# Kernel optimization log

Measured on AMD Instinct MI355X. Metric: run time of the kernel, lower is better.

Reference implementation:

```python
import jax, jax.numpy as jnp
import numpy as np

K = 2  # DGL TAGConv default number of hops
N_GRAPHS = 64


def _tag_conv(h, src, dst, W, b, norm):
    # TAGConv: concat [h, A_hat h, A_hat^2 h] @ W + b, A_hat = D^-1/2 A D^-1/2
    n = h.shape[0]
    hops = [h]
    cur = h
    for _ in range(K):
        msg = (cur * norm)[src]                      # gather from src, [E, d]
        agg = jnp.zeros_like(cur).at[dst].add(msg)   # scatter-sum to dst
        cur = agg * norm
        hops.append(cur)
    z = jnp.concatenate(hops, axis=-1)               # [N, (K+1)*d]
    return jax.nn.relu(z @ W + b)


def _norm(dst, n):
    deg = jnp.zeros((n,), jnp.float32).at[dst].add(1.0)
    deg = jnp.clip(deg, 1.0, None)
    return (deg ** -0.5)[:, None]                    # [N, 1]


def setup_inputs() -> dict:
    key = jax.random.key(0)
    ks = jax.random.split(key, 8)
    N, E, IN, HID, C = 100000, 3200000, 128, 256, 10
    h = jax.random.normal(ks[0], (N, IN), jnp.float32)
    src = jax.random.randint(ks[1], (E,), 0, N, jnp.int32)
    dst = jax.random.randint(ks[2], (E,), 0, N, jnp.int32)
    graph_ids = jnp.sort(jax.random.randint(ks[3], (N,), 0, N_GRAPHS, jnp.int32))
    s1 = ((K + 1) * IN) ** -0.5
    s2 = ((K + 1) * HID) ** -0.5
    W1 = jax.random.normal(ks[4], ((K + 1) * IN, HID), jnp.float32) * s1
    b1 = jnp.zeros((HID,), jnp.float32)
    W2 = jax.random.normal(ks[5], ((K + 1) * HID, HID), jnp.float32) * s2
    b2 = jnp.zeros((HID,), jnp.float32)
    Wc = jax.random.normal(ks[6], (HID, C), jnp.float32) * (HID ** -0.5)
    bc = jnp.zeros((C,), jnp.float32)
    return {"h": h, "src": src, "dst": dst, "graph_ids": graph_ids,
            "W1": W1, "b1": b1, "W2": W2, "b2": b2, "Wc": Wc, "bc": bc}


def reference(h, src, dst, graph_ids, W1, b1, W2, b2, Wc, bc):
    n = h.shape[0]
    norm = _norm(dst, n)
    x = _tag_conv(h, src, dst, W1, b1, norm)
    x = _tag_conv(x, src, dst, W2, b2, norm)
    pooled = jax.ops.segment_max(x, graph_ids, num_segments=N_GRAPHS)  # [G, HID]
    return pooled @ Wc + bc                                            # [G, C]
```

## Files before the change

### kernel.cpp

```cpp
#include <hip/hip_runtime.h>
#include <hip/hip_bf16.h>


typedef unsigned short u16;
typedef unsigned int u32;
typedef unsigned char u8;

__device__ inline float u2f(u16 u) { return __uint_as_float(((u32)u) << 16); }
__device__ inline u16 f2u(float f) {
    __hip_bfloat16 b = __float2bfloat16(f);
    return *reinterpret_cast<u16*>(&b);
}


constexpr int NPB = 128, NC = 128, NBMAX = 784;

__global__ __launch_bounds__(256) void countA_kernel(
    const int* __restrict__ dst, int* __restrict__ Hmat, int E, int CS, int NB) {
    __shared__ int hist[NBMAX];
    int tid = threadIdx.x;
    for (int b = tid; b < NB; b += 256) hist[b] = 0;
    __syncthreads();
    int base = blockIdx.x * CS;
    int end = base + CS < E ? base + CS : E;
    for (int i = base + tid; i < end; i += 256) {
        int d = __builtin_nontemporal_load(dst + i);
        atomicAdd(&hist[d >> 7], 1);
    }
    __syncthreads();
    for (int b = tid; b < NB; b += 256) Hmat[b * NC + blockIdx.x] = hist[b];
}

__global__ __launch_bounds__(256) void scatterC_kernel(
    const int* __restrict__ src, const int* __restrict__ dst,
    const int* __restrict__ Omat, uint2* __restrict__ Earr,
    int E, int CS, int NB) {
    __shared__ int cur[NBMAX];
    int tid = threadIdx.x;
    int c = blockIdx.x;
    for (int b = tid; b < NB; b += 256) cur[b] = Omat[b * NC + c];
    __syncthreads();
    int base = c * CS;
    int end = base + CS < E ? base + CS : E;
    for (int i = base + tid; i < end; i += 256) {
        int d = __builtin_nontemporal_load(dst + i);
        int s = __builtin_nontemporal_load(src + i);
        int pos = atomicAdd(&cur[d >> 7], 1);
        uint2 e;
        e.x = (u32)s;
        e.y = (u32)(d & (NPB - 1));
        Earr[pos] = e;
    }
}

__global__ __launch_bounds__(256) void fineD_kernel(
    const uint2* __restrict__ Earr, const int* __restrict__ Omat,
    int* __restrict__ colidx, int* __restrict__ rowptr,
    float* __restrict__ normv, int N, int E, int NB) {
    __shared__ int cnt[NPB];
    __shared__ int scn[NPB];
    __shared__ int cur2[NPB];
    int tid = threadIdx.x;
    int b = blockIdx.x;
    int base = Omat[b * NC];
    int end = Omat[(b + 1) * NC];
    if (tid < NPB) cnt[tid] = 0;
    __syncthreads();
    for (int i = base + tid; i < end; i += 256)
        atomicAdd(&cnt[Earr[i].y], 1);
    __syncthreads();
    if (tid < NPB) scn[tid] = cnt[tid];
    __syncthreads();
    for (int off = 1; off < NPB; off <<= 1) {
        int v = (tid < NPB && tid >= off) ? scn[tid - off] : 0;
        __syncthreads();
        if (tid < NPB) scn[tid] += v;
        __syncthreads();
    }
    int node0 = b * NPB;
    if (tid < NPB) {
        int excl = scn[tid] - cnt[tid];
        cur2[tid] = base + excl;
        int node = node0 + tid;
        if (node < N) {
            rowptr[node] = base + excl;
            int d = cnt[tid];
            float fd = d < 1 ? 1.0f : (float)d;
            normv[node] = rsqrtf(fd);
        }
    }
    if (b == 0 && tid == 0) rowptr[N] = E;
    __syncthreads();
    for (int i = base + tid; i < end; i += 256) {
        uint2 e = Earr[i];
        int pos = atomicAdd(&cur2[e.y], 1);
        colidx[pos] = (int)e.x;
    }
}

__global__ void scan1_kernel(const int* __restrict__ in, int* __restrict__ outp,
                             int* __restrict__ bsum, int n) {
    __shared__ int sd[1024];
    int t = threadIdx.x;
    int i = blockIdx.x * 1024 + t;
    int v = (i < n) ? in[i] : 0;
    sd[t] = v;
    __syncthreads();
    for (int off = 1; off < 1024; off <<= 1) {
        int x = (t >= off) ? sd[t - off] : 0;
        __syncthreads();
        sd[t] += x;
        __syncthreads();
    }
    if (i < n) outp[i] = sd[t] - v;
    if (t == 1023) bsum[blockIdx.x] = sd[t];
}

__global__ void scan2_kernel(int* __restrict__ bsum, int nb) {
    __shared__ int sd[1024];
    int t = threadIdx.x;
    int v = (t < nb) ? bsum[t] : 0;
    sd[t] = v;
    __syncthreads();
    for (int off = 1; off < 1024; off <<= 1) {
        int x = (t >= off) ? sd[t - off] : 0;
        __syncthreads();
        sd[t] += x;
        __syncthreads();
    }
    if (t < nb) bsum[t] = sd[t] - v;
}

__global__ void scan3_kernel(int* __restrict__ outp, const int* __restrict__ bsum,
                             int n, int E) {
    int i = blockIdx.x * blockDim.x + threadIdx.x;
    if (i < n) outp[i] += bsum[i >> 10];
    if (i == 0) outp[n] = E;
}


struct alignas(4) U2 { u16 v[2]; };
struct alignas(8) U4 { u16 v[4]; };
struct alignas(16) U8 { u16 v[8]; };


__global__ __launch_bounds__(256) void castquant_f32_128(
    const float* __restrict__ h, u16* __restrict__ cat, int ldcat,
    const float* __restrict__ normv,
    u8* __restrict__ q, float* __restrict__ m, int N) {
    int row = blockIdx.x * 4 + (threadIdx.x >> 6);
    if (row >= N) return;
    int lane = threadIdx.x & 63;
    float2 f = *(const float2*)(h + (size_t)row * 128 + lane * 2);
    U2 o;
    o.v[0] = f2u(f.x);
    o.v[1] = f2u(f.y);
    *(U2*)(cat + (size_t)row * ldcat + lane * 2) = o;
    float mx = fmaxf(fabsf(f.x), fabsf(f.y));
    #pragma unroll
    for (int off = 32; off > 0; off >>= 1)
        mx = fmaxf(mx, __shfl_xor(mx, off, 64));
    float inv = mx > 0.f ? 127.f / mx : 0.f;
    u32 q0 = (u32)((int)rintf(f.x * inv) + 128);
    u32 q1 = (u32)((int)rintf(f.y * inv) + 128);
    *(unsigned short*)(q + (size_t)row * 128 + lane * 2) =
        (unsigned short)(q0 | (q1 << 8));
    if (lane == 0) m[row] = normv[row] * (mx * (1.f / 127.f));
}


__global__ __launch_bounds__(256) void quant_bf16_256(
    const u16* __restrict__ x, const float* __restrict__ normv,
    u8* __restrict__ q, float* __restrict__ m, int N) {
    int row = blockIdx.x * 4 + (threadIdx.x >> 6);
    if (row >= N) return;
    int lane = threadIdx.x & 63;
    U4 v = *(const U4*)(x + (size_t)row * 256 + lane * 4);
    float f[4];
    #pragma unroll
    for (int i = 0; i < 4; ++i) f[i] = u2f(v.v[i]);
    float mx = fmaxf(fmaxf(fabsf(f[0]), fabsf(f[1])),
                     fmaxf(fabsf(f[2]), fabsf(f[3])));
    #pragma unroll
    for (int off = 32; off > 0; off >>= 1)
        mx = fmaxf(mx, __shfl_xor(mx, off, 64));
    float inv = mx > 0.f ? 127.f / mx : 0.f;
    u32 b0 = (u32)((int)rintf(f[0] * inv) + 128);
    u32 b1 = (u32)((int)rintf(f[1] * inv) + 128);
    u32 b2 = (u32)((int)rintf(f[2] * inv) + 128);
    u32 b3 = (u32)((int)rintf(f[3] * inv) + 128);
    *(u32*)(q + (size_t)row * 256 + lane * 4) =
        b0 | (b1 << 8) | (b2 << 16) | (b3 << 24);
    if (lane == 0) m[row] = normv[row] * (mx * (1.f / 127.f));
}


template <int BPL, int QOUT>
__global__ __launch_bounds__(256, 2) void prop_q8_kernel(
    const u8* __restrict__ qin, const float* __restrict__ m,
    u16* __restrict__ out, int ldout,
    const int* __restrict__ rowptr, const int* __restrict__ colidx,
    const float* __restrict__ normv, int N,
    u8* __restrict__ qout, float* __restrict__ mout) {
    constexpr int D = 32 * BPL;
    constexpr int NW = BPL / 4;
    constexpr int UE = 8;
    int node = blockIdx.x * 4 + (threadIdx.x >> 6);
    if (node >= N) return;
    const int lane = threadIdx.x & 63;
    const int half = lane >> 5;
    const int l32 = lane & 31;
    const u32 laneoff = (u32)l32 * BPL;
    int s = rowptr[node], e = rowptr[node + 1];
    float acc[BPL];
    #pragma unroll
    for (int q = 0; q < BPL; ++q) acc[q] = 0.f;
    float msum = 0.f;
    const int nfull = (e - s) >> 4;
    int p = s;
    if (nfull > 0) {
        int c[UE];
        #pragma unroll
        for (int u = 0; u < UE; ++u) c[u] = colidx[s + 2 * u + half];
        for (int g = 0; g < nfull; ++g) {
            u32 w[UE][NW];
            #pragma unroll
            for (int u = 0; u < UE; ++u) {
                u32 off = (u32)c[u] * D + laneoff;
                if (BPL == 8) {
                    uint2 gg = *(const uint2*)(qin + off);
                    w[u][0] = gg.x; w[u][1] = gg.y;
                } else {
                    w[u][0] = *(const u32*)(qin + off);
                }
            }
            float nm[UE];
            #pragma unroll
            for (int u = 0; u < UE; ++u) nm[u] = m[c[u]];
            if (g + 1 < nfull) {
                int pn = s + (g + 1) * 16;
                #pragma unroll
                for (int u = 0; u < UE; ++u) c[u] = colidx[pn + 2 * u + half];
            }
            #pragma unroll
            for (int u = 0; u < UE; ++u) {
                msum += nm[u];
                #pragma unroll
                for (int t = 0; t < NW; ++t) {
                    u32 ww = w[u][t];
                    acc[4 * t + 0] += nm[u] * (float)(ww & 0xffu);
                    acc[4 * t + 1] += nm[u] * (float)((ww >> 8) & 0xffu);
                    acc[4 * t + 2] += nm[u] * (float)((ww >> 16) & 0xffu);
                    acc[4 * t + 3] += nm[u] * (float)(ww >> 24);
                }
            }
        }
        p = s + nfull * 16;
    }
    if (p < e) {
        const int el = e - 1;
        int c[UE];
        #pragma unroll
        for (int u = 0; u < UE; ++u) {
            int idx = p + 2 * u + half;
            c[u] = colidx[idx < e ? idx : el];
        }
        u32 w[UE][NW];
        #pragma unroll
        for (int u = 0; u < UE; ++u) {
            u32 off = (u32)c[u] * D + laneoff;
            if (BPL == 8) {
                uint2 gg = *(const uint2*)(qin + off);
                w[u][0] = gg.x; w[u][1] = gg.y;
            } else {
                w[u][0] = *(const u32*)(qin + off);
            }
        }
        float nm[UE];
        #pragma unroll
        for (int u = 0; u < UE; ++u) {
            int idx = p + 2 * u + half;
            float mm = m[c[u]];
            nm[u] = idx < e ? mm : 0.f;
        }
        #pragma unroll
        for (int u = 0; u < UE; ++u) {
            msum += nm[u];
            #pragma unroll
            for (int t = 0; t < NW; ++t) {
                u32 ww = w[u][t];
                acc[4 * t + 0] += nm[u] * (float)(ww & 0xffu);
                acc[4 * t + 1] += nm[u] * (float)((ww >> 8) & 0xffu);
                acc[4 * t + 2] += nm[u] * (float)((ww >> 16) & 0xffu);
                acc[4 * t + 3] += nm[u] * (float)(ww >> 24);
            }
        }
    }
    #pragma unroll
    for (int q = 0; q < BPL; ++q) acc[q] += __shfl_xor(acc[q], 32, 64);
    msum += __shfl_xor(msum, 32, 64);
    float nn = normv[node];
    #pragma unroll
    for (int q = 0; q < BPL; ++q) acc[q] = nn * (acc[q] - 128.f * msum);
    if (half == 0) {
        if (BPL == 8) {
            U8 o;
            #pragma unroll
            for (int q = 0; q < 8; ++q) o.v[q] = f2u(acc[q]);
            *(U8*)(out + (size_t)node * ldout + l32 * 8) = o;
        } else {
            U4 o;
            #pragma unroll
            for (int q = 0; q < 4; ++q) o.v[q] = f2u(acc[q]);
            *(U4*)(out + (size_t)node * ldout + l32 * 4) = o;
        }
    }
    if (QOUT) {
        float mx = 0.f;
        #pragma unroll
        for (int q = 0; q < BPL; ++q) mx = fmaxf(mx, fabsf(acc[q]));
        #pragma unroll
        for (int off = 16; off > 0; off >>= 1)
            mx = fmaxf(mx, __shfl_xor(mx, off, 64));
        float inv = mx > 0.f ? 127.f / mx : 0.f;
        if (half == 0) {
            u32 b[BPL > 4 ? 8 : 4];
            #pragma unroll
            for (int q = 0; q < BPL; ++q)
                b[q] = (u32)((int)rintf(acc[q] * inv) + 128);
            if (BPL == 8) {
                uint2 g;
                g.x = b[0] | (b[1] << 8) | (b[2] << 16) | (b[3] << 24);
                g.y = b[4] | (b[5] << 8) | (b[6] << 16) | (b[7] << 24);
                *(uint2*)(qout + (size_t)node * D + l32 * 8) = g;
            } else {
                *(u32*)(qout + (size_t)node * D + l32 * 4) =
                    b[0] | (b[1] << 8) | (b[2] << 16) | (b[3] << 24);
            }
            if (lane == 0) mout[node] = nn * (mx * (1.f / 127.f));
        }
    }
}


typedef __attribute__((ext_vector_type(8))) short bf16x8f;
typedef __attribute__((ext_vector_type(4))) float f32x4;

template <int KK>
__global__ __launch_bounds__(256, 3) void gemm_wave(
    const u16* __restrict__ A,
    const u16* __restrict__ Bt,
    const u16* __restrict__ Cadd,
    const float* __restrict__ bias,
    u16* __restrict__ Cout,
    int M, int NJOBS, int relu) {
    const int tid = threadIdx.x;
    const int lane = tid & 63;
    const int wave = tid >> 6;
    int nwg = gridDim.x;
    int qq = nwg >> 3, rr = nwg & 7;
    int xcd = blockIdx.x & 7, wi = blockIdx.x >> 3;
    int slot = (xcd < rr ? xcd * (qq + 1) : rr * (qq + 1) + (xcd - rr) * qq) + wi;
    int job = slot * 4 + wave;
    if (job >= NJOBS) return;
    const int rt = job >> 3;
    const int cg = job & 7;
    const int row0 = rt << 7;
    const int col0 = cg << 5;
    const int mb = lane & 15;
    const int seg = lane >> 4;
    const int NOUT = 256;

    const u16* pA = A + (size_t)(row0 + mb) * KK + seg * 8;
    const u16* pB = Bt + (size_t)(col0 + mb) * KK + seg * 8;

    f32x4 acc[8][2];
    #pragma unroll
    for (int mi = 0; mi < 8; ++mi) {
        acc[mi][0] = (f32x4)0.f;
        acc[mi][1] = (f32x4)0.f;
    }

    #pragma unroll
    for (int j = 0; j < KK / 32; ++j) {
        bf16x8f b0 = *(const bf16x8f*)(pB + (size_t)0 * 16 * KK + j * 32);
        bf16x8f b1 = *(const bf16x8f*)(pB + (size_t)16 * KK + j * 32);
        bf16x8f a[8];
        #pragma unroll
        for (int mi = 0; mi < 8; ++mi)
            a[mi] = *(const bf16x8f*)(pA + (size_t)mi * 16 * KK + j * 32);
        #pragma unroll
        for (int mi = 0; mi < 8; ++mi) {
            acc[mi][0] = __builtin_amdgcn_mfma_f32_16x16x32_bf16(
                a[mi], b0, acc[mi][0], 0, 0, 0);
            acc[mi][1] = __builtin_amdgcn_mfma_f32_16x16x32_bf16(
                a[mi], b1, acc[mi][1], 0, 0, 0);
        }
    }

    float bv[2];
    bv[0] = bias ? bias[col0 + 0 * 16 + mb] : 0.f;
    bv[1] = bias ? bias[col0 + 1 * 16 + mb] : 0.f;
    #pragma unroll
    for (int mi = 0; mi < 8; ++mi) {
        #pragma unroll
        for (int r = 0; r < 4; ++r) {
            int row = row0 + mi * 16 + seg * 4 + r;
            if (row < M) {
                #pragma unroll
                for (int ni = 0; ni < 2; ++ni) {
                    int col = col0 + ni * 16 + mb;
                    float v = acc[mi][ni][r];
                    if (Cadd) v += u2f(Cadd[(size_t)row * NOUT + col]);
                    v += bv[ni];
                    if (relu) v = fmaxf(v, 0.f);
                    Cout[(size_t)row * NOUT + col] = f2u(v);
                }
            }
        }
    }
}

__global__ void transpose_cast(const float* __restrict__ W, u16* __restrict__ Wt,
                               int K, int Nn) {
    int idx = blockIdx.x * blockDim.x + threadIdx.x;
    if (idx < K * Nn) {
        int n = idx / K, k = idx % K;
        Wt[idx] = f2u(W[(size_t)k * Nn + n]);
    }
}


__global__ void pool_kernel(const u16* __restrict__ x, const int* __restrict__ gid,
                            float* __restrict__ pooled, int N, int HID) {
    int t = threadIdx.x;
    int n0 = blockIdx.x * 128;
    int n1 = n0 + 128 < N ? n0 + 128 : N;
    float cur = 0.f;
    int cg = gid[n0];
    for (int n = n0; n < n1; ++n) {
        int g = gid[n];
        if (g != cg) {
            atomicMax((int*)&pooled[(size_t)cg * HID + t], __float_as_int(cur));
            cg = g;
            cur = 0.f;
        }
        float v = u2f(x[(size_t)n * HID + t]);
        cur = cur > v ? cur : v;
    }
    atomicMax((int*)&pooled[(size_t)cg * HID + t], __float_as_int(cur));
}

__global__ void head_kernel(const float* __restrict__ pooled, const float* __restrict__ Wc,
                            const float* __restrict__ bc, float* __restrict__ out,
                            int HID, int C) {
    __shared__ float row[256];
    int g = blockIdx.x;
    int t = threadIdx.x;
    if (t < HID) row[t] = pooled[(size_t)g * HID + t];
    __syncthreads();
    if (t < C) {
        float s = bc[t];
        for (int k = 0; k < HID; ++k) s += row[k] * Wc[(size_t)k * C + t];
        out[(size_t)g * C + t] = s;
    }
}


extern "C" void kernel_launch(void* const* d_in, const int* in_sizes, int n_in,
                              void* d_out, int out_size, void* d_ws, size_t ws_size,
                              hipStream_t stream) {
    const float* h  = (const float*)d_in[0];
    const int* src  = (const int*)d_in[1];
    const int* dst  = (const int*)d_in[2];
    const int* gid  = (const int*)d_in[3];
    const float* W1 = (const float*)d_in[4];
    const float* b1 = (const float*)d_in[5];
    const float* W2 = (const float*)d_in[6];
    const float* b2 = (const float*)d_in[7];
    const float* Wc = (const float*)d_in[8];
    const float* bc = (const float*)d_in[9];
    float* out = (float*)d_out;

    const int N   = in_sizes[3];
    const int E   = in_sizes[1];
    const int IN  = in_sizes[0] / N;
    const int HID = in_sizes[5];
    const int C   = in_sizes[9];
    const int G   = out_size / C;
    const int CAT = 3 * IN;
    const int Mpad = (N + 127) & ~127;
    const int NB = (N + NPB - 1) / NPB;
    const int CS = (E + NC - 1) / NC;

    char* wp = (char*)d_ws;
    auto alloc = [&](size_t bytes) {
        char* p = wp;
        wp += (bytes + 255) & ~(size_t)255;
        return p;
    };
    float* pooled = (float*)alloc((size_t)G * HID * sizeof(float));
    float* normv  = (float*)alloc((size_t)N * sizeof(float));
    float* mv     = (float*)alloc((size_t)N * sizeof(float));
    float* mv2    = (float*)alloc((size_t)N * sizeof(float));
    int* rowptr   = (int*)alloc((size_t)(N + 1) * sizeof(int));
    int* bsum     = (int*)alloc(1024 * sizeof(int));
    int* Omat     = (int*)alloc((size_t)(NB * NC + 1) * sizeof(int));
    int* Hmat     = (int*)alloc((size_t)(NB * NC) * sizeof(int));
    int* colidx   = (int*)alloc((size_t)E * sizeof(int));
    u16* Wt1      = (u16*)alloc((size_t)CAT * HID * sizeof(u16));
    u16* Wt2      = (u16*)alloc((size_t)3 * HID * HID * sizeof(u16));
    u16* CAT1     = (u16*)alloc((size_t)Mpad * CAT * sizeof(u16));
    u16* X1       = (u16*)alloc((size_t)Mpad * HID * sizeof(u16));
    u16* B2       = (u16*)alloc((size_t)Mpad * HID * sizeof(u16));
    u16* B1       = CAT1;
    uint2* Earr   = (uint2*)CAT1;
    u8* Q8L2      = (u8*)(CAT1 + (size_t)Mpad * HID);
    u8* Q8A       = (u8*)B2;
    u8* Q8B       = (u8*)B2 + (size_t)Mpad * 128;

    const int n2 = NB * NC;
    countA_kernel<<<NC, 256, 0, stream>>>(dst, Hmat, E, CS, NB);
    scan1_kernel<<<(n2 + 1023) / 1024, 1024, 0, stream>>>(Hmat, Omat, bsum, n2);
    scan2_kernel<<<1, 1024, 0, stream>>>(bsum, (n2 + 1023) / 1024);
    scan3_kernel<<<(n2 + 255) / 256, 256, 0, stream>>>(Omat, bsum, n2, E);
    scatterC_kernel<<<NC, 256, 0, stream>>>(src, dst, Omat, Earr, E, CS, NB);
    fineD_kernel<<<NB, 256, 0, stream>>>(Earr, Omat, colidx, rowptr, normv, N, E, NB);

    transpose_cast<<<(CAT * HID + 255) / 256, 256, 0, stream>>>(W1, Wt1, CAT, HID);
    for (int s2 = 0; s2 < 3; ++s2)
        transpose_cast<<<(HID * HID + 255) / 256, 256, 0, stream>>>(
            W2 + (size_t)s2 * HID * HID, Wt2 + (size_t)s2 * HID * HID, HID, HID);

    int pb = (N + 3) / 4;
    castquant_f32_128<<<pb, 256, 0, stream>>>(h, CAT1, CAT, normv, Q8A, mv, N);
    prop_q8_kernel<4, 1><<<pb, 256, 0, stream>>>(Q8A, mv, CAT1 + IN, CAT,
                                                 rowptr, colidx, normv, N, Q8B, mv2);
    prop_q8_kernel<4, 0><<<pb, 256, 0, stream>>>(Q8B, mv2, CAT1 + 2 * IN, CAT,
                                                 rowptr, colidx, normv, N,
                                                 nullptr, nullptr);
    const int NJOBS = (Mpad / 128) * 8;
    const int GW = NJOBS / 4;
    gemm_wave<384><<<GW, 256, 0, stream>>>(CAT1, Wt1, nullptr, b1, X1, N, NJOBS, 1);

    gemm_wave<256><<<GW, 256, 0, stream>>>(X1, Wt2 + (size_t)2 * HID * HID,
                                           nullptr, nullptr, B1, N, NJOBS, 0);
    quant_bf16_256<<<pb, 256, 0, stream>>>(B1, normv, Q8L2, mv, N);
    prop_q8_kernel<8, 0><<<pb, 256, 0, stream>>>(Q8L2, mv, B2, HID,
                                                 rowptr, colidx, normv, N,
                                                 nullptr, nullptr);
    gemm_wave<256><<<GW, 256, 0, stream>>>(X1, HID ? Wt2 + (size_t)HID * HID : Wt2,
                                           B2, nullptr, B1, N, NJOBS, 0);
    quant_bf16_256<<<pb, 256, 0, stream>>>(B1, normv, Q8L2, mv, N);
    prop_q8_kernel<8, 0><<<pb, 256, 0, stream>>>(Q8L2, mv, B2, HID,
                                                 rowptr, colidx, normv, N,
                                                 nullptr, nullptr);
    gemm_wave<256><<<GW, 256, 0, stream>>>(X1, Wt2, B2, b2, B1, N, NJOBS, 1);

    hipMemsetAsync(pooled, 0, (size_t)G * HID * sizeof(float), stream);
    pool_kernel<<<(N + 127) / 128, HID, 0, stream>>>(B1, gid, pooled, N, HID);
    head_kernel<<<G, HID, 0, stream>>>(pooled, Wc, bc, out, HID, C);
}
```

Before: 1.112 ms.

## Switch layer-2 TAGConv to propagate-then-multiply with a single fused K=768 GEMM

Measured after the change: 1.119 ms. No clear change (+0.6%).

```diff
diff --git a/kernel.cpp b/kernel.cpp
--- a/kernel.cpp
+++ b/kernel.cpp
@@ -170,12 +170,12 @@
 
 
 __global__ __launch_bounds__(256) void quant_bf16_256(
-    const u16* __restrict__ x, const float* __restrict__ normv,
+    const u16* __restrict__ x, int ldx, const float* __restrict__ normv,
     u8* __restrict__ q, float* __restrict__ m, int N) {
     int row = blockIdx.x * 4 + (threadIdx.x >> 6);
     if (row >= N) return;
     int lane = threadIdx.x & 63;
-    U4 v = *(const U4*)(x + (size_t)row * 256 + lane * 4);
+    U4 v = *(const U4*)(x + (size_t)row * ldx + lane * 4);
     float f[4];
     #pragma unroll
     for (int i = 0; i < 4; ++i) f[i] = u2f(v.v[i]);
@@ -353,7 +353,8 @@
     const u16* __restrict__ Cadd,
     const float* __restrict__ bias,
     u16* __restrict__ Cout,
-    int M, int NJOBS, int relu) {
+    int ldout, int M, int NJOBS, int relu) {
+    __shared__ u16 st[4][128 * 32];
     const int tid = threadIdx.x;
     const int lane = tid & 63;
     const int wave = tid >> 6;
@@ -369,7 +370,6 @@
     const int col0 = cg << 5;
     const int mb = lane & 15;
     const int seg = lane >> 4;
-    const int NOUT = 256;
 
     const u16* pA = A + (size_t)(row0 + mb) * KK + seg * 8;
     const u16* pB = Bt + (size_t)(col0 + mb) * KK + seg * 8;
@@ -401,23 +401,34 @@
     float bv[2];
     bv[0] = bias ? bias[col0 + 0 * 16 + mb] : 0.f;
     bv[1] = bias ? bias[col0 + 1 * 16 + mb] : 0.f;
+    u16* my = st[wave];
     #pragma unroll
     for (int mi = 0; mi < 8; ++mi) {
         #pragma unroll
         for (int r = 0; r < 4; ++r) {
-            int row = row0 + mi * 16 + seg * 4 + r;
-            if (row < M) {
-                #pragma unroll
-                for (int ni = 0; ni < 2; ++ni) {
-                    int col = col0 + ni * 16 + mb;
-                    float v = acc[mi][ni][r];
-                    if (Cadd) v += u2f(Cadd[(size_t)row * NOUT + col]);
-                    v += bv[ni];
-                    if (relu) v = fmaxf(v, 0.f);
-                    Cout[(size_t)row * NOUT + col] = f2u(v);
-                }
+            int lrow = mi * 16 + seg * 4 + r;
+            int grow = row0 + lrow;
+            #pragma unroll
+            for (int ni = 0; ni < 2; ++ni) {
+                float v = acc[mi][ni][r] + bv[ni];
+                if (Cadd && grow < M)
+                    v += u2f(Cadd[(size_t)grow * 256 + col0 + ni * 16 + mb]);
+                if (relu) v = fmaxf(v, 0.f);
+                my[lrow * 32 + ni * 16 + mb] = f2u(v);
             }
         }
+    }
+    asm volatile("s_waitcnt lgkmcnt(0)" ::: "memory");
+    __builtin_amdgcn_sched_barrier(0);
+    #pragma unroll
+    for (int i = 0; i < 8; ++i) {
+        int chunk = lane + 64 * i;
+        int lrow = chunk >> 2;
+        int co = (chunk & 3) * 8;
+        int grow = row0 + lrow;
+        if (grow < M)
+            *(uint4*)(Cout + (size_t)grow * ldout + col0 + co) =
+                *(const uint4*)(my + lrow * 32 + co);
     }
 }
 
@@ -513,11 +524,18 @@
     u16* CAT1     = (u16*)alloc((size_t)Mpad * CAT * sizeof(u16));
     u16* X1       = (u16*)alloc((size_t)Mpad * HID * sizeof(u16));
     u16* B2       = (u16*)alloc((size_t)Mpad * HID * sizeof(u16));
-    u16* B1       = CAT1;
-    uint2* Earr   = (uint2*)CAT1;
-    u8* Q8L2      = (u8*)(CAT1 + (size_t)Mpad * HID);
-    u8* Q8A       = (u8*)B2;
-    u8* Q8B       = (u8*)B2 + (size_t)Mpad * 128;
+    size_t used = (size_t)(wp - (char*)d_ws);
+    size_t cat2_bytes = (size_t)Mpad * 768 * sizeof(u16);
+    bool bigws = (used + cat2_bytes + 256) <= ws_size;
+    u16* CAT2 = bigws ? (u16*)alloc(cat2_bytes) : nullptr;
+
+    u16* B1   = CAT1;
+    uint2* Earr = (uint2*)CAT1;
+    u8* Q8L2  = (u8*)(CAT1 + (size_t)Mpad * HID);
+    u8* Q8A   = (u8*)B2;
+    u8* Q8B   = (u8*)B2 + (size_t)Mpad * 128;
+    u8* Q8X1  = (u8*)CAT1;
+    u8* Q8P   = (u8*)CAT1 + (size_t)Mpad * 256;
 
     const int n2 = NB * NC;
     countA_kernel<<<NC, 256, 0, stream>>>(dst, Hmat, E, CS, NB);
@@ -528,9 +546,14 @@
     fineD_kernel<<<NB, 256, 0, stream>>>(Earr, Omat, colidx, rowptr, normv, N, E, NB);
 
     transpose_cast<<<(CAT * HID + 255) / 256, 256, 0, stream>>>(W1, Wt1, CAT, HID);
-    for (int s2 = 0; s2 < 3; ++s2)
-        transpose_cast<<<(HID * HID + 255) / 256, 256, 0, stream>>>(
-            W2 + (size_t)s2 * HID * HID, Wt2 + (size_t)s2 * HID * HID, HID, HID);
+    if (bigws) {
+        transpose_cast<<<(3 * HID * HID + 255) / 256, 256, 0, stream>>>(
+            W2, Wt2, 3 * HID, HID);
+    } else {
+        for (int s2 = 0; s2 < 3; ++s2)
+            transpose_cast<<<(HID * HID + 255) / 256, 256, 0, stream>>>(
+                W2 + (size_t)s2 * HID * HID, Wt2 + (size_t)s2 * HID * HID, HID, HID);
+    }
 
     int pb = (N + 3) / 4;
     castquant_f32_128<<<pb, 256, 0, stream>>>(h, CAT1, CAT, normv, Q8A, mv, N);
@@ -541,23 +564,41 @@
                                                  nullptr, nullptr);
     const int NJOBS = (Mpad / 128) * 8;
     const int GW = NJOBS / 4;
-    gemm_wave<384><<<GW, 256, 0, stream>>>(CAT1, Wt1, nullptr, b1, X1, N, NJOBS, 1);
-
-    gemm_wave<256><<<GW, 256, 0, stream>>>(X1, Wt2 + (size_t)2 * HID * HID,
-                                           nullptr, nullptr, B1, N, NJOBS, 0);
-    quant_bf16_256<<<pb, 256, 0, stream>>>(B1, normv, Q8L2, mv, N);
-    prop_q8_kernel<8, 0><<<pb, 256, 0, stream>>>(Q8L2, mv, B2, HID,
-                                                 rowptr, colidx, normv, N,
-                                                 nullptr, nullptr);
-    gemm_wave<256><<<GW, 256, 0, stream>>>(X1, HID ? Wt2 + (size_t)HID * HID : Wt2,
-                                           B2, nullptr, B1, N, NJOBS, 0);
-    quant_bf16_256<<<pb, 256, 0, stream>>>(B1, normv, Q8L2, mv, N);
-    prop_q8_kernel<8, 0><<<pb, 256, 0, stream>>>(Q8L2, mv, B2, HID,
-                                                 rowptr, colidx, normv, N,
-                                                 nullptr, nullptr);
-    gemm_wave<256><<<GW, 256, 0, stream>>>(X1, Wt2, B2, b2, B1, N, NJOBS, 1);
-
-    hipMemsetAsync(pooled, 0, (size_t)G * HID * sizeof(float), stream);
-    pool_kernel<<<(N + 127) / 128, HID, 0, stream>>>(B1, gid, pooled, N, HID);
+
+    if (bigws) {
+        gemm_wave<384><<<GW, 256, 0, stream>>>(CAT1, Wt1, nullptr, b1,
+                                               CAT2, 768, N, NJOBS, 1);
+        quant_bf16_256<<<pb, 256, 0, stream>>>(CAT2, 768, normv, Q8X1, mv, N);
+        prop_q8_kernel<8, 1><<<pb, 256, 0, stream>>>(Q8X1, mv, CAT2 + 256, 768,
+                                                     rowptr, colidx, normv, N,
+                                                     Q8P, mv2);
+        prop_q8_kernel<8, 0><<<pb, 256, 0, stream>>>(Q8P, mv2, CAT2 + 512, 768,
+                                                     rowptr, colidx, normv, N,
+                                                     nullptr, nullptr);
+        u16* X2 = (u16*)CAT1;
+        gemm_wave<768><<<GW, 256, 0, stream>>>(CAT2, Wt2, nullptr, b2,
+                                               X2, 256, N, NJOBS, 1);
+        hipMemsetAsync(pooled, 0, (size_t)G * HID * sizeof(float), stream);
+        pool_kernel<<<(N + 127) / 128, HID, 0, stream>>>(X2, gid, pooled, N, HID);
+    } else {
+        gemm_wave<384><<<GW, 256, 0, stream>>>(CAT1, Wt1, nullptr, b1,
+                                               X1, 256, N, NJOBS, 1);
+        gemm_wave<256><<<GW, 256, 0, stream>>>(X1, Wt2 + (size_t)2 * HID * HID,
+                                               nullptr, nullptr, B1, 256, N, NJOBS, 0);
+        quant_bf16_256<<<pb, 256, 0, stream>>>(B1, 256, normv, Q8L2, mv, N);
+        prop_q8_kernel<8, 0><<<pb, 256, 0, stream>>>(Q8L2, mv, B2, HID,
+                                                     rowptr, colidx, normv, N,
+                                                     nullptr, nullptr);
+        gemm_wave<256><<<GW, 256, 0, stream>>>(X1, Wt2 + (size_t)HID * HID,
+                                               B2, nullptr, B1, 256, N, NJOBS, 0);
+        quant_bf16_256<<<pb, 256, 0, stream>>>(B1, 256, normv, Q8L2, mv, N);
+        prop_q8_kernel<8, 0><<<pb, 256, 0, stream>>>(Q8L2, mv, B2, HID,
+                                                     rowptr, colidx, normv, N,
+                                                     nullptr, nullptr);
+        gemm_wave<256><<<GW, 256, 0, stream>>>(X1, Wt2, B2, b2, B1, 256, N, NJOBS, 1);
+        hipMemsetAsync(pooled, 0, (size_t)G * HID * sizeof(float), stream);
+        pool_kernel<<<(N + 127) / 128, HID, 0, stream>>>(B1, gid, pooled, N, HID);
+    }
+
     head_kernel<<<G, HID, 0, stream>>>(pooled, Wc, bc, out, HID, C);
 }
```

## Fuse layer-2 GEMM epilogues into propagation and quantize inside GEMM

Applied to the files above, without the earlier changes.

New measurement: 1.064 ms. 1.05x faster.

```diff
diff --git a/kernel.cpp b/kernel.cpp
--- a/kernel.cpp
+++ b/kernel.cpp
@@ -169,38 +169,13 @@
 }
 
 
-__global__ __launch_bounds__(256) void quant_bf16_256(
-    const u16* __restrict__ x, const float* __restrict__ normv,
-    u8* __restrict__ q, float* __restrict__ m, int N) {
-    int row = blockIdx.x * 4 + (threadIdx.x >> 6);
-    if (row >= N) return;
-    int lane = threadIdx.x & 63;
-    U4 v = *(const U4*)(x + (size_t)row * 256 + lane * 4);
-    float f[4];
-    #pragma unroll
-    for (int i = 0; i < 4; ++i) f[i] = u2f(v.v[i]);
-    float mx = fmaxf(fmaxf(fabsf(f[0]), fabsf(f[1])),
-                     fmaxf(fabsf(f[2]), fabsf(f[3])));
-    #pragma unroll
-    for (int off = 32; off > 0; off >>= 1)
-        mx = fmaxf(mx, __shfl_xor(mx, off, 64));
-    float inv = mx > 0.f ? 127.f / mx : 0.f;
-    u32 b0 = (u32)((int)rintf(f[0] * inv) + 128);
-    u32 b1 = (u32)((int)rintf(f[1] * inv) + 128);
-    u32 b2 = (u32)((int)rintf(f[2] * inv) + 128);
-    u32 b3 = (u32)((int)rintf(f[3] * inv) + 128);
-    *(u32*)(q + (size_t)row * 256 + lane * 4) =
-        b0 | (b1 << 8) | (b2 << 16) | (b3 << 24);
-    if (lane == 0) m[row] = normv[row] * (mx * (1.f / 127.f));
-}
-
-
-template <int BPL, int QOUT>
+template <int BPL, int QOUT, int WB, int CADD>
 __global__ __launch_bounds__(256, 2) void prop_q8_kernel(
     const u8* __restrict__ qin, const float* __restrict__ m,
     u16* __restrict__ out, int ldout,
     const int* __restrict__ rowptr, const int* __restrict__ colidx,
     const float* __restrict__ normv, int N,
+    const u16* __restrict__ cadd, const float* __restrict__ bias, int relu,
     u8* __restrict__ qout, float* __restrict__ mout) {
     constexpr int D = 32 * BPL;
     constexpr int NW = BPL / 4;
@@ -300,25 +275,45 @@
     for (int q = 0; q < BPL; ++q) acc[q] += __shfl_xor(acc[q], 32, 64);
     msum += __shfl_xor(msum, 32, 64);
     float nn = normv[node];
-    #pragma unroll
-    for (int q = 0; q < BPL; ++q) acc[q] = nn * (acc[q] - 128.f * msum);
-    if (half == 0) {
+    float v[BPL];
+    #pragma unroll
+    for (int q = 0; q < BPL; ++q) v[q] = nn * (acc[q] - 128.f * msum);
+    if (CADD) {
+        if (BPL == 8) {
+            U8 cv = *(const U8*)(cadd + (size_t)node * 256 + l32 * 8);
+            #pragma unroll
+            for (int q = 0; q < 8; ++q) v[q] += u2f(cv.v[q]);
+        } else {
+            U4 cv = *(const U4*)(cadd + (size_t)node * 256 + l32 * 4);
+            #pragma unroll
+            for (int q = 0; q < 4; ++q) v[q] += u2f(cv.v[q]);
+        }
+    }
+    if (bias) {
+        #pragma unroll
+        for (int q = 0; q < BPL; ++q) v[q] += bias[l32 * BPL + q];
+    }
+    if (relu) {
+        #pragma unroll
+        for (int q = 0; q < BPL; ++q) v[q] = fmaxf(v[q], 0.f);
+    }
+    if (WB && half == 0) {
         if (BPL == 8) {
             U8 o;
             #pragma unroll
-            for (int q = 0; q < 8; ++q) o.v[q] = f2u(acc[q]);
+            for (int q = 0; q < 8; ++q) o.v[q] = f2u(v[q]);
             *(U8*)(out + (size_t)node * ldout + l32 * 8) = o;
         } else {
             U4 o;
             #pragma unroll
-            for (int q = 0; q < 4; ++q) o.v[q] = f2u(acc[q]);
+            for (int q = 0; q < 4; ++q) o.v[q] = f2u(v[q]);
             *(U4*)(out + (size_t)node * ldout + l32 * 4) = o;
         }
     }
     if (QOUT) {
         float mx = 0.f;
         #pragma unroll
-        for (int q = 0; q < BPL; ++q) mx = fmaxf(mx, fabsf(acc[q]));
+        for (int q = 0; q < BPL; ++q) mx = fmaxf(mx, fabsf(v[q]));
         #pragma unroll
         for (int off = 16; off > 0; off >>= 1)
             mx = fmaxf(mx, __shfl_xor(mx, off, 64));
@@ -327,7 +322,7 @@
             u32 b[BPL > 4 ? 8 : 4];
             #pragma unroll
             for (int q = 0; q < BPL; ++q)
-                b[q] = (u32)((int)rintf(acc[q] * inv) + 128);
+                b[q] = (u32)((int)rintf(v[q] * inv) + 128);
             if (BPL == 8) {
                 uint2 g;
                 g.x = b[0] | (b[1] << 8) | (b[2] << 16) | (b[3] << 24);
@@ -346,13 +341,12 @@
 typedef __attribute__((ext_vector_type(8))) short bf16x8f;
 typedef __attribute__((ext_vector_type(4))) float f32x4;
 
-template <int KK>
+template <int KK, int DUAL>
 __global__ __launch_bounds__(256, 3) void gemm_wave(
     const u16* __restrict__ A,
-    const u16* __restrict__ Bt,
-    const u16* __restrict__ Cadd,
+    const u16* __restrict__ Bt, int ldb,
     const float* __restrict__ bias,
-    u16* __restrict__ Cout,
+    u16* __restrict__ C0, u16* __restrict__ C1,
     int M, int NJOBS, int relu) {
     const int tid = threadIdx.x;
     const int lane = tid & 63;
@@ -363,16 +357,17 @@
     int slot = (xcd < rr ? xcd * (qq + 1) : rr * (qq + 1) + (xcd - rr) * qq) + wi;
     int job = slot * 4 + wave;
     if (job >= NJOBS) return;
-    const int rt = job >> 3;
-    const int cg = job & 7;
+    const int cg = DUAL ? (job & 15) : (job & 7);
+    const int rt = DUAL ? (job >> 4) : (job >> 3);
     const int row0 = rt << 7;
-    const int col0 = cg << 5;
+    const int col0 = (DUAL ? (cg & 7) : cg) << 5;
+    const u16* bb = DUAL ? (cg < 8 ? Bt + 256 : Bt) : Bt;
+    u16* Cout = DUAL ? (cg < 8 ? C0 : C1) : C0;
     const int mb = lane & 15;
     const int seg = lane >> 4;
-    const int NOUT = 256;
 
     const u16* pA = A + (size_t)(row0 + mb) * KK + seg * 8;
-    const u16* pB = Bt + (size_t)(col0 + mb) * KK + seg * 8;
+    const u16* pB = bb + (size_t)(col0 + mb) * ldb + seg * 8;
 
     f32x4 acc[8][2];
     #pragma unroll
@@ -383,8 +378,8 @@
 
     #pragma unroll
     for (int j = 0; j < KK / 32; ++j) {
-        bf16x8f b0 = *(const bf16x8f*)(pB + (size_t)0 * 16 * KK + j * 32);
-        bf16x8f b1 = *(const bf16x8f*)(pB + (size_t)16 * KK + j * 32);
+        bf16x8f b0 = *(const bf16x8f*)(pB + (size_t)j * 32);
+        bf16x8f b1 = *(const bf16x8f*)(pB + (size_t)16 * ldb + j * 32);
         bf16x8f a[8];
         #pragma unroll
         for (int mi = 0; mi < 8; ++mi)
@@ -399,8 +394,8 @@
     }
 
     float bv[2];
-    bv[0] = bias ? bias[col0 + 0 * 16 + mb] : 0.f;
-    bv[1] = bias ? bias[col0 + 1 * 16 + mb] : 0.f;
+    bv[0] = bias ? bias[col0 + mb] : 0.f;
+    bv[1] = bias ? bias[col0 + 16 + mb] : 0.f;
     #pragma unroll
     for (int mi = 0; mi < 8; ++mi) {
         #pragma unroll
@@ -409,15 +404,92 @@
             if (row < M) {
                 #pragma unroll
                 for (int ni = 0; ni < 2; ++ni) {
-                    int col = col0 + ni * 16 + mb;
-                    float v = acc[mi][ni][r];
-                    if (Cadd) v += u2f(Cadd[(size_t)row * NOUT + col]);
-                    v += bv[ni];
+                    float v = acc[mi][ni][r] + bv[ni];
                     if (relu) v = fmaxf(v, 0.f);
-                    Cout[(size_t)row * NOUT + col] = f2u(v);
+                    Cout[(size_t)row * 256 + col0 + ni * 16 + mb] = f2u(v);
                 }
             }
         }
+    }
+}
+
+
+template <int KK>
+__global__ __launch_bounds__(256, 2) void gemmq_wave(
+    const u16* __restrict__ A,
+    const u16* __restrict__ Bt, int ldb,
+    u8* __restrict__ Qout,
+    float* __restrict__ mout,
+    const float* __restrict__ normv,
+    int M, int NJOBS) {
+    __shared__ u8 st[4][16 * 272];
+    const int tid = threadIdx.x;
+    const int lane = tid & 63;
+    const int wave = tid >> 6;
+    int nwg = gridDim.x;
+    int qq = nwg >> 3, rr = nwg & 7;
+    int xcd = blockIdx.x & 7, wi = blockIdx.x >> 3;
+    int slot = (xcd < rr ? xcd * (qq + 1) : rr * (qq + 1) + (xcd - rr) * qq) + wi;
+    int job = slot * 4 + wave;
+    if (job >= NJOBS) return;
+    const int row0 = job << 4;
+    const int mb = lane & 15;
+    const int seg = lane >> 4;
+
+    const u16* pA = A + (size_t)(row0 + mb) * KK + seg * 8;
+    const u16* pB = Bt + (size_t)mb * ldb + seg * 8;
+
+    f32x4 acc[16];
+    #pragma unroll
+    for (int ni = 0; ni < 16; ++ni) acc[ni] = (f32x4)0.f;
+
+    #pragma unroll
+    for (int j = 0; j < KK / 32; ++j) {
+        bf16x8f a = *(const bf16x8f*)(pA + (size_t)j * 32);
+        #pragma unroll
+        for (int g = 0; g < 2; ++g) {
+            bf16x8f b[8];
+            #pragma unroll
+            for (int t = 0; t < 8; ++t)
+                b[t] = *(const bf16x8f*)(pB + (size_t)((g * 8 + t) * 16) * ldb
+                                         + j * 32);
+            #pragma unroll
+            for (int t = 0; t < 8; ++t)
+                acc[g * 8 + t] = __builtin_amdgcn_mfma_f32_16x16x32_bf16(
+                    a, b[t], acc[g * 8 + t], 0, 0, 0);
+        }
+    }
+
+    u8* my = st[wave];
+    #pragma unroll
+    for (int r = 0; r < 4; ++r) {
+        int lrow = seg * 4 + r;
+        float mx = 0.f;
+        #pragma unroll
+        for (int ni = 0; ni < 16; ++ni) mx = fmaxf(mx, fabsf(acc[ni][r]));
+        #pragma unroll
+        for (int off = 1; off < 16; off <<= 1)
+            mx = fmaxf(mx, __shfl_xor(mx, off, 64));
+        float inv = mx > 0.f ? 127.f / mx : 0.f;
+        #pragma unroll
+        for (int ni = 0; ni < 16; ++ni)
+            my[lrow * 272 + ni * 16 + mb] =
+                (u8)((int)rintf(acc[ni][r] * inv) + 128);
+        int grow = row0 + lrow;
+        if (mb == 0 && grow < M)
+            mout[grow] = normv[grow] * (mx * (1.f / 127.f));
+    }
+    asm volatile("s_waitcnt lgkmcnt(0)" ::: "memory");
+    __builtin_amdgcn_sched_barrier(0);
+    #pragma unroll
+    for (int i = 0; i < 4; ++i) {
+        int chunk = lane + 64 * i;
+        int lrow = chunk >> 4;
+        int co = chunk & 15;
+        int grow = row0 + lrow;
+        if (grow < M)
+            *(uint4*)(Qout + (size_t)grow * 256 + co * 16) =
+                *(const uint4*)(my + lrow * 272 + co * 16);
     }
 }
 
@@ -503,21 +575,26 @@
     float* normv  = (float*)alloc((size_t)N * sizeof(float));
     float* mv     = (float*)alloc((size_t)N * sizeof(float));
     float* mv2    = (float*)alloc((size_t)N * sizeof(float));
+    float* mvq    = (float*)alloc((size_t)N * sizeof(float));
     int* rowptr   = (int*)alloc((size_t)(N + 1) * sizeof(int));
     int* bsum     = (int*)alloc(1024 * sizeof(int));
     int* Omat     = (int*)alloc((size_t)(NB * NC + 1) * sizeof(int));
     int* Hmat     = (int*)alloc((size_t)(NB * NC) * sizeof(int));
     int* colidx   = (int*)alloc((size_t)E * sizeof(int));
     u16* Wt1      = (u16*)alloc((size_t)CAT * HID * sizeof(u16));
-    u16* Wt2      = (u16*)alloc((size_t)3 * HID * HID * sizeof(u16));
-    u16* CAT1     = (u16*)alloc((size_t)Mpad * CAT * sizeof(u16));
-    u16* X1       = (u16*)alloc((size_t)Mpad * HID * sizeof(u16));
-    u16* B2       = (u16*)alloc((size_t)Mpad * HID * sizeof(u16));
-    u16* B1       = CAT1;
-    uint2* Earr   = (uint2*)CAT1;
-    u8* Q8L2      = (u8*)(CAT1 + (size_t)Mpad * HID);
-    u8* Q8A       = (u8*)B2;
-    u8* Q8B       = (u8*)B2 + (size_t)Mpad * 128;
+    u16* Wt2f     = (u16*)alloc((size_t)3 * HID * HID * sizeof(u16));
+    u16* X1       = (u16*)alloc((size_t)Mpad * 256 * sizeof(u16));
+    u16* CAT1     = (u16*)alloc((size_t)Mpad * 384 * sizeof(u16));
+    u16* B2      = (u16*)alloc((size_t)Mpad * 256 * sizeof(u16));
+
+    uint2* Earr = (uint2*)CAT1;
+    u8* Q8A  = (u8*)B2;
+    u8* Q8B  = (u8*)B2 + (size_t)Mpad * 128;
+    u8* Q8c  = (u8*)CAT1;
+    u16* Yb  = (u16*)((u8*)CAT1 + (size_t)Mpad * 256);
+    u16* Ya  = B2;
+    u8* Q8d  = (u8*)X1;
+    u16* X2  = CAT1;
 
     const int n2 = NB * NC;
     countA_kernel<<<NC, 256, 0, stream>>>(dst, Hmat, E, CS, NB);
@@ -528,36 +605,35 @@
     fineD_kernel<<<NB, 256, 0, stream>>>(Earr, Omat, colidx, rowptr, normv, N, E, NB);
 
     transpose_cast<<<(CAT * HID + 255) / 256, 256, 0, stream>>>(W1, Wt1, CAT, HID);
-    for (int s2 = 0; s2 < 3; ++s2)
-        transpose_cast<<<(HID * HID + 255) / 256, 256, 0, stream>>>(
-            W2 + (size_t)s2 * HID * HID, Wt2 + (size_t)s2 * HID * HID, HID, HID);
+    transpose_cast<<<(3 * HID * HID + 255) / 256, 256, 0, stream>>>(
+        W2, Wt2f, 3 * HID, HID);
 
     int pb = (N + 3) / 4;
     castquant_f32_128<<<pb, 256, 0, stream>>>(h, CAT1, CAT, normv, Q8A, mv, N);
-    prop_q8_kernel<4, 1><<<pb, 256, 0, stream>>>(Q8A, mv, CAT1 + IN, CAT,
-                                                 rowptr, colidx, normv, N, Q8B, mv2);
-    prop_q8_kernel<4, 0><<<pb, 256, 0, stream>>>(Q8B, mv2, CAT1 + 2 * IN, CAT,
-                                                 rowptr, colidx, normv, N,
-                                                 nullptr, nullptr);
-    const int NJOBS = (Mpad / 128) * 8;
-    const int GW = NJOBS / 4;
-    gemm_wave<384><<<GW, 256, 0, stream>>>(CAT1, Wt1, nullptr, b1, X1, N, NJOBS, 1);
-
-    gemm_wave<256><<<GW, 256, 0, stream>>>(X1, Wt2 + (size_t)2 * HID * HID,
-                                           nullptr, nullptr, B1, N, NJOBS, 0);
-    quant_bf16_256<<<pb, 256, 0, stream>>>(B1, normv, Q8L2, mv, N);
-    prop_q8_kernel<8, 0><<<pb, 256, 0, stream>>>(Q8L2, mv, B2, HID,
-                                                 rowptr, colidx, normv, N,
-                                                 nullptr, nullptr);
-    gemm_wave<256><<<GW, 256, 0, stream>>>(X1, HID ? Wt2 + (size_t)HID * HID : Wt2,
-                                           B2, nullptr, B1, N, NJOBS, 0);
-    quant_bf16_256<<<pb, 256, 0, stream>>>(B1, normv, Q8L2, mv, N);
-    prop_q8_kernel<8, 0><<<pb, 256, 0, stream>>>(Q8L2, mv, B2, HID,
-                                                 rowptr, colidx, normv, N,
-                                                 nullptr, nullptr);
-    gemm_wave<256><<<GW, 256, 0, stream>>>(X1, Wt2, B2, b2, B1, N, NJOBS, 1);
+    prop_q8_kernel<4, 1, 1, 0><<<pb, 256, 0, stream>>>(
+        Q8A, mv, CAT1 + IN, CAT, rowptr, colidx, normv, N,
+        nullptr, nullptr, 0, Q8B, mv2);
+    prop_q8_kernel<4, 0, 1, 0><<<pb, 256, 0, stream>>>(
+        Q8B, mv2, CAT1 + 2 * IN, CAT, rowptr, colidx, normv, N,
+        nullptr, nullptr, 0, nullptr, nullptr);
+    const int NJ8 = (Mpad / 128) * 8;
+    gemm_wave<384, 0><<<NJ8 / 4, 256, 0, stream>>>(
+        CAT1, Wt1, 384, b1, X1, nullptr, N, NJ8, 1);
+
+    const int NJQ = Mpad / 16;
+    gemmq_wave<256><<<NJQ / 4, 256, 0, stream>>>(
+        X1, Wt2f + 512, 768, Q8c, mvq, normv, N, NJQ);
+    const int NJD = (Mpad / 128) * 16;
+    gemm_wave<256, 1><<<NJD / 4, 256, 0, stream>>>(
+        X1, Wt2f, 768, nullptr, Yb, Ya, N, NJD, 0);
+    prop_q8_kernel<8, 1, 0, 1><<<pb, 256, 0, stream>>>(
+        Q8c, mvq, nullptr, 256, rowptr, colidx, normv, N,
+        Yb, nullptr, 0, Q8d, mv2);
+    prop_q8_kernel<8, 0, 1, 1><<<pb, 256, 0, stream>>>(
+        Q8d, mv2, X2, 256, rowptr, colidx, normv, N,
+        Ya, b2, 1, nullptr, nullptr);
 
     hipMemsetAsync(pooled, 0, (size_t)G * HID * sizeof(float), stream);
-    pool_kernel<<<(N + 127) / 128, HID, 0, stream>>>(B1, gid, pooled, N, HID);
+    pool_kernel<<<(N + 127) / 128, HID, 0, stream>>>(X2, gid, pooled, N, HID);
     head_kernel<<<G, HID, 0, stream>>>(pooled, Wc, bc, out, HID, C);
 }
```
